# Kernel optimization log

Hardware: AMD Instinct MI355X
Metric: run time of the kernel (lower is better)

## Reference

```python
import jax, jax.numpy as jnp
import numpy as np

NUM_HASHES = 10
GROUP = 2
K = 5


def _strip_att(x, conv_w, rvecs, horizontal):
    # x: [n, c, h, w]; conv_w: [group*k, c]; rvecs: [num_hashes, c]
    n, c, h, w = x.shape
    hw = h * w
    pad = K // 2

    # ---- LSH group selection (vectorized, no python batch loop) ----
    x_flat = x.reshape(n, c, hw).transpose(0, 2, 1)          # [n, hw, c]
    proj = jnp.einsum('ntc,hc->nth', x_flat, rvecs)          # [n, hw, num_hashes]
    codes = (proj > 0).astype(jnp.float32)
    pow2 = jnp.power(2.0, jnp.arange(NUM_HASHES, dtype=jnp.float32))
    dec = codes @ pow2                                       # [n, hw]
    order = jnp.argsort(dec, axis=1)                         # [n, hw]
    sorted_t = jnp.take_along_axis(x_flat, order[:, :, None], axis=1)  # [n, hw, c]

    # select_best_group: batch element with largest L2 norm, shared by all
    norms = jnp.linalg.norm(sorted_t.reshape(n, -1), axis=1)  # [n]
    best = jnp.argmax(norms)
    best_group = jnp.take(sorted_t, best, axis=0)             # [hw, c]
    bg = jnp.broadcast_to(best_group.T.reshape(1, c, h, w), (n, c, h, w))

    # ---- sigmoid-gated dynamic strip filter (1x1 conv) ----
    filt = jnp.einsum('oc,nchw->nohw', conv_w, bg)            # [n, group*K, h, w]
    filt = jax.nn.sigmoid(filt).reshape(n, GROUP, 1, K, hw)

    # ---- unfold (im2col) along the strip axis, reflect-padded ----
    if horizontal:
        xp = jnp.pad(x, ((0, 0), (0, 0), (0, 0), (pad, pad)), mode='reflect')
        windows = jnp.stack([xp[:, :, :, i:i + w] for i in range(K)], axis=2)  # [n,c,K,h,w]
    else:
        xp = jnp.pad(x, ((0, 0), (0, 0), (pad, pad), (0, 0)), mode='reflect')
        windows = jnp.stack([xp[:, :, i:i + h, :] for i in range(K)], axis=2)  # [n,c,K,h,w]
    xr = windows.reshape(n, GROUP, c // GROUP, K, hw)

    out = jnp.sum(xr * filt, axis=3).reshape(n, c, h, w)
    return out


def setup_inputs() -> dict:
    key = jax.random.key(0)
    ks = jax.random.split(key, 7)
    n, c, h, w = 4, 64, 256, 256
    return {
        'x': jax.random.normal(ks[0], (n, c, h, w), dtype=jnp.float32),
        'conv_h_w': jax.random.normal(ks[1], (GROUP * K, c), dtype=jnp.float32) * 0.1,
        'conv_w_w': jax.random.normal(ks[2], (GROUP * K, c), dtype=jnp.float32) * 0.1,
        'rvecs_h': jax.random.normal(ks[3], (NUM_HASHES, c), dtype=jnp.float32),
        'rvecs_w': jax.random.normal(ks[4], (NUM_HASHES, c), dtype=jnp.float32),
        'gamma': jax.random.normal(ks[5], (c,), dtype=jnp.float32),
        'beta': jax.random.normal(ks[6], (c,), dtype=jnp.float32),
    }


def reference(x, conv_h_w, conv_w_w, rvecs_h, rvecs_w, gamma, beta):
    out = _strip_att(x, conv_h_w, rvecs_h, horizontal=True)
    out = _strip_att(out, conv_w_w, rvecs_w, horizontal=False)
    return gamma[None, :, None, None] * out + x * beta[None, :, None, None]
```

## Files before the change

### kernel.cpp

```cpp
#include <hip/hip_runtime.h>

#define NB 4
#define C 64
#define H 256
#define W 256
#define HW (H * W)
#define NH 10
#define KK 5
#define NBINS 1024
#define CHUNK 256
#define NCHUNK (HW / CHUNK)

__global__ __launch_bounds__(256) void sumsq_kernel(const float* __restrict__ x,
                                                    float* __restrict__ part) {
    int bid = blockIdx.x;
    int b = bid >> 8, ch = bid & 255;
    const float4* p = reinterpret_cast<const float4*>(x + (size_t)b * C * HW) + (size_t)ch * 4096;
    float s = 0.f;
    for (int i = threadIdx.x; i < 4096; i += 256) {
        float4 v = p[i];
        s += v.x * v.x + v.y * v.y + v.z * v.z + v.w * v.w;
    }
    __shared__ float red[256];
    red[threadIdx.x] = s;
    __syncthreads();
    for (int off = 128; off; off >>= 1) {
        if (threadIdx.x < off) red[threadIdx.x] += red[threadIdx.x + off];
        __syncthreads();
    }
    if (threadIdx.x == 0) part[bid] = red[0];
}

__global__ __launch_bounds__(256) void hash_kernel(const float* __restrict__ Xall,
                                                   const float* __restrict__ part,
                                                   int per_batch,
                                                   const float* __restrict__ rvecs,
                                                   const float* __restrict__ cwg,
                                                   float* __restrict__ filtU,
                                                   int* __restrict__ dec,
                                                   int* __restrict__ hist) {
    __shared__ float tile[32][CHUNK + 4];
    __shared__ float rv[NH * C];
    __shared__ float cw[NH * C];
    __shared__ int lhist[NBINS];
    __shared__ float4 red4[256];
    int t = threadIdx.x;
    for (int i = t; i < NH * C; i += 256) { rv[i] = rvecs[i]; cw[i] = cwg[i]; }
    for (int i = t; i < NBINS; i += 256) lhist[i] = 0;

    float4 ss = make_float4(0.f, 0.f, 0.f, 0.f);
    int q4 = per_batch >> 2;
    for (int i = t; i < q4; i += 256) {
        float4 a = *reinterpret_cast<const float4*>(part + 0 * per_batch + i * 4);
        float4 b = *reinterpret_cast<const float4*>(part + 1 * per_batch + i * 4);
        float4 c = *reinterpret_cast<const float4*>(part + 2 * per_batch + i * 4);
        float4 d = *reinterpret_cast<const float4*>(part + 3 * per_batch + i * 4);
        ss.x += a.x + a.y + a.z + a.w;
        ss.y += b.x + b.y + b.z + b.w;
        ss.z += c.x + c.y + c.z + c.w;
        ss.w += d.x + d.y + d.z + d.w;
    }
    red4[t] = ss;
    __syncthreads();
    for (int off = 128; off; off >>= 1) {
        if (t < off) {
            red4[t].x += red4[t + off].x;
            red4[t].y += red4[t + off].y;
            red4[t].z += red4[t + off].z;
            red4[t].w += red4[t + off].w;
        }
        __syncthreads();
    }
    float4 nm = red4[0];
    float nv[NB] = {nm.x, nm.y, nm.z, nm.w};
    int best = 0;
    float m = nv[0];
#pragma unroll
    for (int i = 1; i < NB; i++)
        if (nv[i] > m) { m = nv[i]; best = i; }

    const float* X = Xall + (size_t)best * C * HW;
    int p0 = blockIdx.x * CHUNK;
    int lane = t & 63, cq = t >> 6;
    float acc[NH], cacc[NH];
#pragma unroll
    for (int h = 0; h < NH; h++) { acc[h] = 0.f; cacc[h] = 0.f; }

    for (int half = 0; half < 2; half++) {
        __syncthreads();
        const float* Xh = X + (size_t)(half * 32) * HW + p0;
#pragma unroll
        for (int rep = 0; rep < 8; rep++) {
            int cl = rep * 4 + cq;
            float4 v = *reinterpret_cast<const float4*>(Xh + (size_t)cl * HW + lane * 4);
            *reinterpret_cast<float4*>(&tile[cl][lane * 4]) = v;
        }
        __syncthreads();
#pragma unroll
        for (int c = 0; c < 32; c++) {
            float v = tile[c][t];
            int ci = half * 32 + c;
#pragma unroll
            for (int h = 0; h < NH; h++) {
                acc[h] += v * rv[h * C + ci];
                cacc[h] += v * cw[h * C + ci];
            }
        }
    }
    int d = 0;
#pragma unroll
    for (int h = 0; h < NH; h++) d |= (acc[h] > 0.f) ? (1 << h) : 0;
    dec[p0 + t] = d;
    atomicAdd(&lhist[d], 1);

    float sg[NH];
#pragma unroll
    for (int h = 0; h < NH; h++) sg[h] = 1.f / (1.f + expf(-cacc[h]));
    float* fu = filtU + (size_t)(p0 + t) * 12;
    *reinterpret_cast<float4*>(fu + 0) = make_float4(sg[0], sg[1], sg[2], sg[3]);
    *reinterpret_cast<float4*>(fu + 4) = make_float4(sg[4], sg[5], sg[6], sg[7]);
    *reinterpret_cast<float4*>(fu + 8) = make_float4(sg[8], sg[9], 0.f, 0.f);

    __syncthreads();
    for (int i = t; i < NBINS; i += 256) hist[(size_t)i * NCHUNK + blockIdx.x] = lhist[i];
}

__global__ __launch_bounds__(256) void scan1_kernel(int* __restrict__ hist,
                                                    int* __restrict__ bintot) {
    int t = threadIdx.x;
    int lane = t & 63;
    int b = blockIdx.x * 4 + (t >> 6);
    int4 v = *reinterpret_cast<int4*>(hist + (size_t)b * NCHUNK + lane * 4);
    int s0 = v.x, s1 = s0 + v.y, s2 = s1 + v.z, s3 = s2 + v.w;
    int s = s3;
#pragma unroll
    for (int off = 1; off < 64; off <<= 1) {
        int nbr = __shfl_up(s, off);
        if (lane >= off) s += nbr;
    }
    int excl = s - s3;
    int4 o;
    o.x = excl;
    o.y = excl + s0;
    o.z = excl + s1;
    o.w = excl + s2;
    *reinterpret_cast<int4*>(hist + (size_t)b * NCHUNK + lane * 4) = o;
    if (lane == 63) bintot[b] = s;
}

__global__ __launch_bounds__(256) void scatter_kernel(const int* __restrict__ dec,
                                                      const int* __restrict__ hist,
                                                      const int* __restrict__ bintot,
                                                      const float* __restrict__ filtU,
                                                      float* __restrict__ filt) {
    __shared__ int boffs[NBINS];
    __shared__ int wtot[4];
    __shared__ int keys[CHUNK];
    int t = threadIdx.x;
    int lane = t & 63;
    int w = t >> 6;
    int4 v = *reinterpret_cast<const int4*>(bintot + t * 4);
    int s0 = v.x, s1 = s0 + v.y, s2 = s1 + v.z, s3 = s2 + v.w;
    int s = s3;
#pragma unroll
    for (int off = 1; off < 64; off <<= 1) {
        int nbr = __shfl_up(s, off);
        if (lane >= off) s += nbr;
    }
    int excl = s - s3;
    if (lane == 63) wtot[w] = s;
    __syncthreads();
    int wbase = 0;
#pragma unroll
    for (int i = 0; i < 4; i++) wbase += (i < w) ? wtot[i] : 0;
    boffs[t * 4 + 0] = wbase + excl;
    boffs[t * 4 + 1] = wbase + excl + s0;
    boffs[t * 4 + 2] = wbase + excl + s1;
    boffs[t * 4 + 3] = wbase + excl + s2;

    int p0 = blockIdx.x * CHUNK;
    int k = dec[p0 + t];
    keys[t] = k;
    __syncthreads();
    int r = 0;
    for (int j = 0; j < t; j++) r += (keys[j] == k) ? 1 : 0;
    int dst = boffs[k] + hist[(size_t)k * NCHUNK + blockIdx.x] + r;

    const float4* fu = reinterpret_cast<const float4*>(filtU + (size_t)(p0 + t) * 12);
    float4 a = fu[0], b4 = fu[1], c4 = fu[2];
    float vv[10] = {a.x, a.y, a.z, a.w, b4.x, b4.y, b4.z, b4.w, c4.x, c4.y};
#pragma unroll
    for (int h = 0; h < NH; h++) filt[(size_t)h * HW + dst] = vv[h];
}

__global__ __launch_bounds__(256) void convh_kernel(const float* __restrict__ X,
                                                    const float* __restrict__ filt,
                                                    float* __restrict__ out1,
                                                    float* __restrict__ part) {
    int bid = blockIdx.x;
    int rb = bid & 63;
    int c = (bid >> 6) & (C - 1);
    int n = bid >> 12;
    int g = c >> 5;
    int t = threadIdx.x;
    int x4 = (t & 63) * 4;
    int y = rb * 4 + (t >> 6);

    const float* src = X + (((size_t)n * C + c) * H + y) * W;
    float4 M = *reinterpret_cast<const float4*>(src + x4);
    float s0, s1, s6, s7;
    if (x4 > 0) {
        float4 L = *reinterpret_cast<const float4*>(src + x4 - 4);
        s0 = L.z; s1 = L.w;
    } else {
        s0 = M.z; s1 = M.y;
    }
    if (x4 < W - 4) {
        float4 R = *reinterpret_cast<const float4*>(src + x4 + 4);
        s6 = R.x; s7 = R.y;
    } else {
        s6 = M.z; s7 = M.y;
    }
    float s[8] = {s0, s1, M.x, M.y, M.z, M.w, s6, s7};

    const float* fb = filt + (size_t)g * KK * HW + (size_t)y * W + x4;
    float4 acc = make_float4(0.f, 0.f, 0.f, 0.f);
#pragma unroll
    for (int k = 0; k < KK; k++) {
        float4 f = *reinterpret_cast<const float4*>(fb + (size_t)k * HW);
        acc.x += s[k] * f.x;
        acc.y += s[k + 1] * f.y;
        acc.z += s[k + 2] * f.z;
        acc.w += s[k + 3] * f.w;
    }
    *reinterpret_cast<float4*>(out1 + (((size_t)n * C + c) * H + y) * W + x4) = acc;

    float ss = acc.x * acc.x + acc.y * acc.y + acc.z * acc.z + acc.w * acc.w;
#pragma unroll
    for (int off = 32; off; off >>= 1) ss += __shfl_down(ss, off);
    __shared__ float wred[4];
    if ((t & 63) == 0) wred[t >> 6] = ss;
    __syncthreads();
    if (t == 0) part[bid] = wred[0] + wred[1] + wred[2] + wred[3];
}

__global__ __launch_bounds__(256) void convv_kernel(const float* __restrict__ out1,
                                                    const float* __restrict__ filt,
                                                    const float* __restrict__ x,
                                                    const float* __restrict__ gamma,
                                                    const float* __restrict__ beta,
                                                    float* __restrict__ out) {
    int bid = blockIdx.x;
    int yc = bid & 3;
    int c = (bid >> 2) & (C - 1);
    int n = bid >> 8;
    int g = c >> 5;
    int t = threadIdx.x;
    int x4 = (t & 63) * 4;
    int ys = yc * 64 + (t >> 6) * 16;

    const float* plane = out1 + ((size_t)n * C + c) * HW;
    float4 win[KK];
#pragma unroll
    for (int i = 0; i < 4; i++) {
        int yy = ys - 2 + i;
        yy = yy < 0 ? -yy : yy;
        win[i] = *reinterpret_cast<const float4*>(plane + (size_t)yy * W + x4);
    }
    float gm = gamma[c], bt = beta[c];
    const float* fgb = filt + (size_t)g * KK * HW;
    for (int dy = 0; dy < 16; dy++) {
        int y = ys + dy;
        int yy = y + 2;
        yy = (yy >= H) ? (2 * H - 2 - yy) : yy;
        win[4] = *reinterpret_cast<const float4*>(plane + (size_t)yy * W + x4);
        const float* fb = fgb + (size_t)y * W + x4;
        float4 acc = make_float4(0.f, 0.f, 0.f, 0.f);
#pragma unroll
        for (int k = 0; k < KK; k++) {
            float4 f = *reinterpret_cast<const float4*>(fb + (size_t)k * HW);
            acc.x += win[k].x * f.x;
            acc.y += win[k].y * f.y;
            acc.z += win[k].z * f.z;
            acc.w += win[k].w * f.w;
        }
        size_t idx = (((size_t)n * C + c) * H + y) * W + x4;
        float4 xv = *reinterpret_cast<const float4*>(x + idx);
        float4 o;
        o.x = gm * acc.x + bt * xv.x;
        o.y = gm * acc.y + bt * xv.y;
        o.z = gm * acc.z + bt * xv.z;
        o.w = gm * acc.w + bt * xv.w;
        *reinterpret_cast<float4*>(out + idx) = o;
#pragma unroll
        for (int k = 0; k < 4; k++) win[k] = win[k + 1];
    }
}

extern "C" void kernel_launch(void* const* d_in, const int* in_sizes, int n_in,
                              void* d_out, int out_size, void* d_ws, size_t ws_size,
                              hipStream_t stream) {
    const float* x      = (const float*)d_in[0];
    const float* conv_h = (const float*)d_in[1];
    const float* conv_w = (const float*)d_in[2];
    const float* rv_h   = (const float*)d_in[3];
    const float* rv_w   = (const float*)d_in[4];
    const float* gamma  = (const float*)d_in[5];
    const float* beta   = (const float*)d_in[6];
    float* out = (float*)d_out;

    char* w = (char*)d_ws;
    size_t off = 0;
    float* out1   = (float*)(w + off); off += (size_t)NB * C * HW * 4;
    float* filtU  = (float*)(w + off); off += (size_t)HW * 12 * 4;
    float* filt   = (float*)(w + off); off += (size_t)NH * HW * 4;
    int*   dec    = (int*)  (w + off); off += (size_t)HW * 4;
    int*   hist   = (int*)  (w + off); off += (size_t)NBINS * NCHUNK * 4;
    int*   bintot = (int*)  (w + off); off += 4096;
    float* part1  = (float*)(w + off); off += (size_t)NB * 256 * 4;
    float* part2  = (float*)(w + off); off += (size_t)NB * 4096 * 4;

    sumsq_kernel<<<NB * 256, 256, 0, stream>>>(x, part1);
    hash_kernel<<<NCHUNK, 256, 0, stream>>>(x, part1, 256, rv_h, conv_h, filtU, dec, hist);
    scan1_kernel<<<NBINS / 4, 256, 0, stream>>>(hist, bintot);
    scatter_kernel<<<NCHUNK, 256, 0, stream>>>(dec, hist, bintot, filtU, filt);
    convh_kernel<<<NB * C * (H / 4), 256, 0, stream>>>(x, filt, out1, part2);

    hash_kernel<<<NCHUNK, 256, 0, stream>>>(out1, part2, 4096, rv_w, conv_w, filtU, dec, hist);
    scan1_kernel<<<NBINS / 4, 256, 0, stream>>>(hist, bintot);
    scatter_kernel<<<NCHUNK, 256, 0, stream>>>(dec, hist, bintot, filtU, filt);
    convv_kernel<<<NB * C * 4, 256, 0, stream>>>(out1, filt, x, gamma, beta, out);
}
```

Baseline: 145.6 us.

## Fuse all stages into one cooperative persistent kernel with grid syncs

Replaces the nine separate kernel launches with a single cooperative persistent kernel that loops over work units per phase and separates phases with grid-wide barriers. The per-phase bodies become device functions sharing reused shared-memory buffers, and the old launch sequence stays as a fallback. The sumsq and hash tiling are retuned to smaller chunks (2048 sumsq units, 8-channel hash tiles) to fit the shared buffer. The aim is to remove launch gaps between the many small phases. The cost is grid.sync overhead, a grid capped at the occupancy limit, and lower occupancy, since the fused kernel holds the largest shared-memory and register footprint of all phases for the whole run.

After: 430.8 us. +196.0%, slower.

```diff
diff --git a/kernel.cpp b/kernel.cpp
--- a/kernel.cpp
+++ b/kernel.cpp
@@ -1,4 +1,7 @@
 #include <hip/hip_runtime.h>
+#include <hip/hip_cooperative_groups.h>
+
+namespace cg = cooperative_groups;
 
 #define NB 4
 #define C 64
@@ -10,44 +13,32 @@
 #define NBINS 1024
 #define CHUNK 256
 #define NCHUNK (HW / CHUNK)
-
-__global__ __launch_bounds__(256) void sumsq_kernel(const float* __restrict__ x,
-                                                    float* __restrict__ part) {
-    int bid = blockIdx.x;
-    int b = bid >> 8, ch = bid & 255;
-    const float4* p = reinterpret_cast<const float4*>(x + (size_t)b * C * HW) + (size_t)ch * 4096;
+#define MAXGRID 2048
+
+
+__device__ __forceinline__ void sumsq_unit(int u, int t, float* smA,
+                                           const float* __restrict__ x,
+                                           float* __restrict__ part1) {
+    int b = u >> 9, ch = u & 511;
+    const float4* p = reinterpret_cast<const float4*>(x + (size_t)b * C * HW) + (size_t)ch * 2048;
     float s = 0.f;
-    for (int i = threadIdx.x; i < 4096; i += 256) {
+    for (int i = t; i < 2048; i += 256) {
         float4 v = p[i];
         s += v.x * v.x + v.y * v.y + v.z * v.z + v.w * v.w;
     }
-    __shared__ float red[256];
-    red[threadIdx.x] = s;
+    smA[t] = s;
     __syncthreads();
     for (int off = 128; off; off >>= 1) {
-        if (threadIdx.x < off) red[threadIdx.x] += red[threadIdx.x + off];
+        if (t < off) smA[t] += smA[t + off];
         __syncthreads();
     }
-    if (threadIdx.x == 0) part[bid] = red[0];
-}
-
-__global__ __launch_bounds__(256) void hash_kernel(const float* __restrict__ Xall,
-                                                   const float* __restrict__ part,
-                                                   int per_batch,
-                                                   const float* __restrict__ rvecs,
-                                                   const float* __restrict__ cwg,
-                                                   float* __restrict__ filtU,
-                                                   int* __restrict__ dec,
-                                                   int* __restrict__ hist) {
-    __shared__ float tile[32][CHUNK + 4];
-    __shared__ float rv[NH * C];
-    __shared__ float cw[NH * C];
-    __shared__ int lhist[NBINS];
-    __shared__ float4 red4[256];
-    int t = threadIdx.x;
-    for (int i = t; i < NH * C; i += 256) { rv[i] = rvecs[i]; cw[i] = cwg[i]; }
-    for (int i = t; i < NBINS; i += 256) lhist[i] = 0;
-
+    if (t == 0) part1[u] = smA[0];
+    __syncthreads();
+}
+
+__device__ __forceinline__ int block_argmax(int t, float* smA,
+                                            const float* __restrict__ part, int per_batch) {
+    float4* red4 = reinterpret_cast<float4*>(smA);
     float4 ss = make_float4(0.f, 0.f, 0.f, 0.f);
     int q4 = per_batch >> 2;
     for (int i = t; i < q4; i += 256) {
@@ -72,34 +63,49 @@
         __syncthreads();
     }
     float4 nm = red4[0];
+    __syncthreads();
     float nv[NB] = {nm.x, nm.y, nm.z, nm.w};
     int best = 0;
     float m = nv[0];
 #pragma unroll
     for (int i = 1; i < NB; i++)
         if (nv[i] > m) { m = nv[i]; best = i; }
+    return best;
+}
+
+__device__ __forceinline__ void hash_phase(int u, int t, float* smA, float* smB,
+        const float* __restrict__ Xall, const float* __restrict__ part, int per_batch,
+        const float* __restrict__ rvecs, const float* __restrict__ cwg,
+        float* __restrict__ filtU, int* __restrict__ dec, int* __restrict__ hist) {
+    float* rv = smB;
+    float* cw = smB + NH * C;
+    int* lhist = reinterpret_cast<int*>(smB + 2 * NH * C);
+    for (int i = t; i < NH * C; i += 256) { rv[i] = rvecs[i]; cw[i] = cwg[i]; }
+    for (int i = t; i < NBINS; i += 256) lhist[i] = 0;
+    int best = block_argmax(t, smA, part, per_batch);
 
     const float* X = Xall + (size_t)best * C * HW;
-    int p0 = blockIdx.x * CHUNK;
-    int lane = t & 63, cq = t >> 6;
+    int p0 = u * CHUNK;
     float acc[NH], cacc[NH];
 #pragma unroll
     for (int h = 0; h < NH; h++) { acc[h] = 0.f; cacc[h] = 0.f; }
-
-    for (int half = 0; half < 2; half++) {
+    float(*tile)[CHUNK + 4] = reinterpret_cast<float(*)[CHUNK + 4]>(smA);
+    for (int s8 = 0; s8 < 8; s8++) {
         __syncthreads();
-        const float* Xh = X + (size_t)(half * 32) * HW + p0;
-#pragma unroll
-        for (int rep = 0; rep < 8; rep++) {
-            int cl = rep * 4 + cq;
-            float4 v = *reinterpret_cast<const float4*>(Xh + (size_t)cl * HW + lane * 4);
+#pragma unroll
+        for (int k = 0; k < 2; k++) {
+            int idx = t + k * 256;
+            int cl = idx >> 6;
+            int lane = idx & 63;
+            float4 v = *reinterpret_cast<const float4*>(
+                X + (size_t)(s8 * 8 + cl) * HW + p0 + lane * 4);
             *reinterpret_cast<float4*>(&tile[cl][lane * 4]) = v;
         }
         __syncthreads();
 #pragma unroll
-        for (int c = 0; c < 32; c++) {
+        for (int c = 0; c < 8; c++) {
             float v = tile[c][t];
-            int ci = half * 32 + c;
+            int ci = s8 * 8 + c;
 #pragma unroll
             for (int h = 0; h < NH; h++) {
                 acc[h] += v * rv[h * C + ci];
@@ -112,7 +118,6 @@
     for (int h = 0; h < NH; h++) d |= (acc[h] > 0.f) ? (1 << h) : 0;
     dec[p0 + t] = d;
     atomicAdd(&lhist[d], 1);
-
     float sg[NH];
 #pragma unroll
     for (int h = 0; h < NH; h++) sg[h] = 1.f / (1.f + expf(-cacc[h]));
@@ -120,16 +125,15 @@
     *reinterpret_cast<float4*>(fu + 0) = make_float4(sg[0], sg[1], sg[2], sg[3]);
     *reinterpret_cast<float4*>(fu + 4) = make_float4(sg[4], sg[5], sg[6], sg[7]);
     *reinterpret_cast<float4*>(fu + 8) = make_float4(sg[8], sg[9], 0.f, 0.f);
-
-    __syncthreads();
-    for (int i = t; i < NBINS; i += 256) hist[(size_t)i * NCHUNK + blockIdx.x] = lhist[i];
-}
-
-__global__ __launch_bounds__(256) void scan1_kernel(int* __restrict__ hist,
-                                                    int* __restrict__ bintot) {
-    int t = threadIdx.x;
+    __syncthreads();
+    for (int i = t; i < NBINS; i += 256) hist[(size_t)i * NCHUNK + u] = lhist[i];
+    __syncthreads();
+}
+
+__device__ __forceinline__ void scan_phase(int u, int t, int* __restrict__ hist,
+                                           int* __restrict__ bintot) {
     int lane = t & 63;
-    int b = blockIdx.x * 4 + (t >> 6);
+    int b = u * 4 + (t >> 6);
     int4 v = *reinterpret_cast<int4*>(hist + (size_t)b * NCHUNK + lane * 4);
     int s0 = v.x, s1 = s0 + v.y, s2 = s1 + v.z, s3 = s2 + v.w;
     int s = s3;
@@ -148,15 +152,13 @@
     if (lane == 63) bintot[b] = s;
 }
 
-__global__ __launch_bounds__(256) void scatter_kernel(const int* __restrict__ dec,
-                                                      const int* __restrict__ hist,
-                                                      const int* __restrict__ bintot,
-                                                      const float* __restrict__ filtU,
-                                                      float* __restrict__ filt) {
-    __shared__ int boffs[NBINS];
-    __shared__ int wtot[4];
-    __shared__ int keys[CHUNK];
-    int t = threadIdx.x;
+__device__ __forceinline__ void scatter_phase(int u, int t, float* smA,
+        const int* __restrict__ dec, const int* __restrict__ hist,
+        const int* __restrict__ bintot, const float* __restrict__ filtU,
+        float* __restrict__ filt) {
+    int* boffs = reinterpret_cast<int*>(smA);
+    int* wtot = boffs + NBINS;
+    int* keys = wtot + 4;
     int lane = t & 63;
     int w = t >> 6;
     int4 v = *reinterpret_cast<const int4*>(bintot + t * 4);
@@ -178,31 +180,29 @@
     boffs[t * 4 + 2] = wbase + excl + s1;
     boffs[t * 4 + 3] = wbase + excl + s2;
 
-    int p0 = blockIdx.x * CHUNK;
+    int p0 = u * CHUNK;
     int k = dec[p0 + t];
     keys[t] = k;
     __syncthreads();
     int r = 0;
     for (int j = 0; j < t; j++) r += (keys[j] == k) ? 1 : 0;
-    int dst = boffs[k] + hist[(size_t)k * NCHUNK + blockIdx.x] + r;
+    int dst = boffs[k] + hist[(size_t)k * NCHUNK + u] + r;
 
     const float4* fu = reinterpret_cast<const float4*>(filtU + (size_t)(p0 + t) * 12);
     float4 a = fu[0], b4 = fu[1], c4 = fu[2];
     float vv[10] = {a.x, a.y, a.z, a.w, b4.x, b4.y, b4.z, b4.w, c4.x, c4.y};
 #pragma unroll
     for (int h = 0; h < NH; h++) filt[(size_t)h * HW + dst] = vv[h];
-}
-
-__global__ __launch_bounds__(256) void convh_kernel(const float* __restrict__ X,
-                                                    const float* __restrict__ filt,
-                                                    float* __restrict__ out1,
-                                                    float* __restrict__ part) {
-    int bid = blockIdx.x;
-    int rb = bid & 63;
-    int c = (bid >> 6) & (C - 1);
-    int n = bid >> 12;
+    __syncthreads();
+}
+
+__device__ __forceinline__ void convh_unit(int u, int t, float* smA,
+        const float* __restrict__ X, const float* __restrict__ filt,
+        float* __restrict__ out1, float* __restrict__ part2) {
+    int rb = u & 63;
+    int c = (u >> 6) & (C - 1);
+    int n = u >> 12;
     int g = c >> 5;
-    int t = threadIdx.x;
     int x4 = (t & 63) * 4;
     int y = rb * 4 + (t >> 6);
 
@@ -238,24 +238,20 @@
     float ss = acc.x * acc.x + acc.y * acc.y + acc.z * acc.z + acc.w * acc.w;
 #pragma unroll
     for (int off = 32; off; off >>= 1) ss += __shfl_down(ss, off);
-    __shared__ float wred[4];
-    if ((t & 63) == 0) wred[t >> 6] = ss;
-    __syncthreads();
-    if (t == 0) part[bid] = wred[0] + wred[1] + wred[2] + wred[3];
-}
-
-__global__ __launch_bounds__(256) void convv_kernel(const float* __restrict__ out1,
-                                                    const float* __restrict__ filt,
-                                                    const float* __restrict__ x,
-                                                    const float* __restrict__ gamma,
-                                                    const float* __restrict__ beta,
-                                                    float* __restrict__ out) {
-    int bid = blockIdx.x;
-    int yc = bid & 3;
-    int c = (bid >> 2) & (C - 1);
-    int n = bid >> 8;
+    if ((t & 63) == 0) smA[t >> 6] = ss;
+    __syncthreads();
+    if (t == 0) part2[u] = smA[0] + smA[1] + smA[2] + smA[3];
+    __syncthreads();
+}
+
+__device__ __forceinline__ void convv_unit(int u, int t,
+        const float* __restrict__ out1, const float* __restrict__ filt,
+        const float* __restrict__ x, const float* __restrict__ gamma,
+        const float* __restrict__ beta, float* __restrict__ out) {
+    int yc = u & 3;
+    int c = (u >> 2) & (C - 1);
+    int n = u >> 8;
     int g = c >> 5;
-    int t = threadIdx.x;
     int x4 = (t & 63) * 4;
     int ys = yc * 64 + (t >> 6) * 16;
 
@@ -297,6 +293,83 @@
     }
 }
 
+__global__ __launch_bounds__(256) void mega_kernel(
+        const float* __restrict__ x, const float* __restrict__ convh_w,
+        const float* __restrict__ convw_w, const float* __restrict__ rvh,
+        const float* __restrict__ rvw, const float* __restrict__ gamma,
+        const float* __restrict__ beta, float* __restrict__ out,
+        float* __restrict__ out1, float* __restrict__ filtU, float* __restrict__ filt,
+        int* __restrict__ dec, int* __restrict__ hist, int* __restrict__ bintot,
+        float* __restrict__ part1, float* __restrict__ part2) {
+    cg::grid_group grid = cg::this_grid();
+    __shared__ __align__(16) float smA[2080];
+    __shared__ __align__(16) float smB[2304];
+    int t = threadIdx.x;
+    int bid = blockIdx.x;
+    int gd = gridDim.x;
+
+    for (int u = bid; u < 2048; u += gd) sumsq_unit(u, t, smA, x, part1);
+    grid.sync();
+    for (int u = bid; u < NCHUNK; u += gd)
+        hash_phase(u, t, smA, smB, x, part1, 512, rvh, convh_w, filtU, dec, hist);
+    grid.sync();
+    for (int u = bid; u < NBINS / 4; u += gd) scan_phase(u, t, hist, bintot);
+    grid.sync();
+    for (int u = bid; u < NCHUNK; u += gd)
+        scatter_phase(u, t, smA, dec, hist, bintot, filtU, filt);
+    grid.sync();
+    for (int u = bid; u < NB * C * (H / 4); u += gd)
+        convh_unit(u, t, smA, x, filt, out1, part2);
+    grid.sync();
+    for (int u = bid; u < NCHUNK; u += gd)
+        hash_phase(u, t, smA, smB, out1, part2, 4096, rvw, convw_w, filtU, dec, hist);
+    grid.sync();
+    for (int u = bid; u < NBINS / 4; u += gd) scan_phase(u, t, hist, bintot);
+    grid.sync();
+    for (int u = bid; u < NCHUNK; u += gd)
+        scatter_phase(u, t, smA, dec, hist, bintot, filtU, filt);
+    grid.sync();
+    for (int u = bid; u < NB * C * 4; u += gd)
+        convv_unit(u, t, out1, filt, x, gamma, beta, out);
+}
+
+__global__ __launch_bounds__(256) void k_sumsq(const float* __restrict__ x,
+                                               float* __restrict__ part1) {
+    __shared__ __align__(16) float smA[256];
+    sumsq_unit(blockIdx.x, threadIdx.x, smA, x, part1);
+}
+__global__ __launch_bounds__(256) void k_hash(const float* __restrict__ Xall,
+        const float* __restrict__ part, int per_batch, const float* __restrict__ rvecs,
+        const float* __restrict__ cwg, float* __restrict__ filtU,
+        int* __restrict__ dec, int* __restrict__ hist) {
+    __shared__ __align__(16) float smA[2080];
+    __shared__ __align__(16) float smB[2304];
+    hash_phase(blockIdx.x, threadIdx.x, smA, smB, Xall, part, per_batch, rvecs, cwg,
+               filtU, dec, hist);
+}
+__global__ __launch_bounds__(256) void k_scan(int* __restrict__ hist,
+                                              int* __restrict__ bintot) {
+    scan_phase(blockIdx.x, threadIdx.x, hist, bintot);
+}
+__global__ __launch_bounds__(256) void k_scatter(const int* __restrict__ dec,
+        const int* __restrict__ hist, const int* __restrict__ bintot,
+        const float* __restrict__ filtU, float* __restrict__ filt) {
+    __shared__ __align__(16) float smA[1312];
+    scatter_phase(blockIdx.x, threadIdx.x, smA, dec, hist, bintot, filtU, filt);
+}
+__global__ __launch_bounds__(256) void k_convh(const float* __restrict__ X,
+        const float* __restrict__ filt, float* __restrict__ out1,
+        float* __restrict__ part2) {
+    __shared__ __align__(16) float smA[4];
+    convh_unit(blockIdx.x, threadIdx.x, smA, X, filt, out1, part2);
+}
+__global__ __launch_bounds__(256) void k_convv(const float* __restrict__ out1,
+        const float* __restrict__ filt, const float* __restrict__ x,
+        const float* __restrict__ gamma, const float* __restrict__ beta,
+        float* __restrict__ out) {
+    convv_unit(blockIdx.x, threadIdx.x, out1, filt, x, gamma, beta, out);
+}
+
 extern "C" void kernel_launch(void* const* d_in, const int* in_sizes, int n_in,
                               void* d_out, int out_size, void* d_ws, size_t ws_size,
                               hipStream_t stream) {
@@ -317,17 +390,39 @@
     int*   dec    = (int*)  (w + off); off += (size_t)HW * 4;
     int*   hist   = (int*)  (w + off); off += (size_t)NBINS * NCHUNK * 4;
     int*   bintot = (int*)  (w + off); off += 4096;
-    float* part1  = (float*)(w + off); off += (size_t)NB * 256 * 4;
+    float* part1  = (float*)(w + off); off += (size_t)NB * 512 * 4;
     float* part2  = (float*)(w + off); off += (size_t)NB * 4096 * 4;
 
-    sumsq_kernel<<<NB * 256, 256, 0, stream>>>(x, part1);
-    hash_kernel<<<NCHUNK, 256, 0, stream>>>(x, part1, 256, rv_h, conv_h, filtU, dec, hist);
-    scan1_kernel<<<NBINS / 4, 256, 0, stream>>>(hist, bintot);
-    scatter_kernel<<<NCHUNK, 256, 0, stream>>>(dec, hist, bintot, filtU, filt);
-    convh_kernel<<<NB * C * (H / 4), 256, 0, stream>>>(x, filt, out1, part2);
-
-    hash_kernel<<<NCHUNK, 256, 0, stream>>>(out1, part2, 4096, rv_w, conv_w, filtU, dec, hist);
-    scan1_kernel<<<NBINS / 4, 256, 0, stream>>>(hist, bintot);
-    scatter_kernel<<<NCHUNK, 256, 0, stream>>>(dec, hist, bintot, filtU, filt);
-    convv_kernel<<<NB * C * 4, 256, 0, stream>>>(out1, filt, x, gamma, beta, out);
-}
+    int dev = 0;
+    (void)hipGetDevice(&dev);
+    int nMP = 0;
+    (void)hipDeviceGetAttribute(&nMP, hipDeviceAttributeMultiprocessorCount, dev);
+    int bpm = 0;
+    hipError_t oe = hipOccupancyMaxActiveBlocksPerMultiprocessor(&bpm, mega_kernel, 256, 0);
+
+    bool coop_ok = false;
+    if (oe == hipSuccess && nMP > 0 && bpm > 0) {
+        int G = nMP * bpm;
+        if (G > MAXGRID) G = MAXGRID;
+        if (G >= 64) {
+            void* args[] = {&x, &conv_h, &conv_w, &rv_h, &rv_w, &gamma, &beta,
+                            &out, &out1, &filtU, &filt, &dec, &hist, &bintot,
+                            &part1, &part2};
+            hipError_t le = hipLaunchCooperativeKernel(
+                reinterpret_cast<void*>(mega_kernel), dim3(G), dim3(256), args, 0, stream);
+            coop_ok = (le == hipSuccess);
+        }
+    }
+
+    if (!coop_ok) {
+        k_sumsq<<<2048, 256, 0, stream>>>(x, part1);
+        k_hash<<<NCHUNK, 256, 0, stream>>>(x, part1, 512, rv_h, conv_h, filtU, dec, hist);
+        k_scan<<<NBINS / 4, 256, 0, stream>>>(hist, bintot);
+        k_scatter<<<NCHUNK, 256, 0, stream>>>(dec, hist, bintot, filtU, filt);
+        k_convh<<<NB * C * (H / 4), 256, 0, stream>>>(x, filt, out1, part2);
+        k_hash<<<NCHUNK, 256, 0, stream>>>(out1, part2, 4096, rv_w, conv_w, filtU, dec, hist);
+        k_scan<<<NBINS / 4, 256, 0, stream>>>(hist, bintot);
+        k_scatter<<<NCHUNK, 256, 0, stream>>>(dec, hist, bintot, filtU, filt);
+        k_convv<<<NB * C * 4, 256, 0, stream>>>(out1, filt, x, gamma, beta, out);
+    }
+}
```

## Split hash projection across 1024 threads and use ballot-based stable rank in scatter

Applied to the files above, without the earlier changes.

The hash kernel now uses 1024-thread blocks. Each quarter of the threads projects 16 channels per pixel, and the partial sums are reduced through shared memory. The scatter kernel replaces its O(n) linear scan for stable rank with per-wave ballot matching on the 10 key bits plus per-wave shared histograms. The sumsq kernel is split into twice as many blocks. These changes target the long serial loops in the hash and scatter kernels, at the cost of more shared-memory traffic and barriers in the hash reduction.

Result: faster. 139.3 us (-4.3%).

```diff
diff --git a/kernel.cpp b/kernel.cpp
--- a/kernel.cpp
+++ b/kernel.cpp
@@ -11,46 +11,43 @@
 #define CHUNK 256
 #define NCHUNK (HW / CHUNK)
 
-__global__ __launch_bounds__(256) void sumsq_kernel(const float* __restrict__ x,
-                                                    float* __restrict__ part) {
-    int bid = blockIdx.x;
-    int b = bid >> 8, ch = bid & 255;
-    const float4* p = reinterpret_cast<const float4*>(x + (size_t)b * C * HW) + (size_t)ch * 4096;
+__global__ __launch_bounds__(256) void k_sumsq(const float* __restrict__ x,
+                                               float* __restrict__ part1) {
+    __shared__ float red[256];
+    int u = blockIdx.x, t = threadIdx.x;
+    int b = u >> 9, ch = u & 511;
+    const float4* p = reinterpret_cast<const float4*>(x + (size_t)b * C * HW) + (size_t)ch * 2048;
     float s = 0.f;
-    for (int i = threadIdx.x; i < 4096; i += 256) {
+    for (int i = t; i < 2048; i += 256) {
         float4 v = p[i];
         s += v.x * v.x + v.y * v.y + v.z * v.z + v.w * v.w;
     }
-    __shared__ float red[256];
-    red[threadIdx.x] = s;
+    red[t] = s;
     __syncthreads();
     for (int off = 128; off; off >>= 1) {
-        if (threadIdx.x < off) red[threadIdx.x] += red[threadIdx.x + off];
+        if (t < off) red[t] += red[t + off];
         __syncthreads();
     }
-    if (threadIdx.x == 0) part[bid] = red[0];
-}
-
-__global__ __launch_bounds__(256) void hash_kernel(const float* __restrict__ Xall,
-                                                   const float* __restrict__ part,
-                                                   int per_batch,
-                                                   const float* __restrict__ rvecs,
-                                                   const float* __restrict__ cwg,
-                                                   float* __restrict__ filtU,
-                                                   int* __restrict__ dec,
-                                                   int* __restrict__ hist) {
-    __shared__ float tile[32][CHUNK + 4];
-    __shared__ float rv[NH * C];
-    __shared__ float cw[NH * C];
+    if (t == 0) part1[u] = red[0];
+}
+
+__global__ __launch_bounds__(1024) void k_hash(const float* __restrict__ Xall,
+                                               const float* __restrict__ part,
+                                               int per_batch,
+                                               const float* __restrict__ rvecs,
+                                               const float* __restrict__ cwg,
+                                               float* __restrict__ filtU,
+                                               int* __restrict__ dec,
+                                               int* __restrict__ hist) {
+    __shared__ __align__(16) float smbuf[256 * 21];
     __shared__ int lhist[NBINS];
-    __shared__ float4 red4[256];
     int t = threadIdx.x;
-    for (int i = t; i < NH * C; i += 256) { rv[i] = rvecs[i]; cw[i] = cwg[i]; }
-    for (int i = t; i < NBINS; i += 256) lhist[i] = 0;
-
+    for (int i = t; i < NBINS; i += 1024) lhist[i] = 0;
+
+    float4* red4 = reinterpret_cast<float4*>(smbuf);
     float4 ss = make_float4(0.f, 0.f, 0.f, 0.f);
     int q4 = per_batch >> 2;
-    for (int i = t; i < q4; i += 256) {
+    for (int i = t; i < q4; i += 1024) {
         float4 a = *reinterpret_cast<const float4*>(part + 0 * per_batch + i * 4);
         float4 b = *reinterpret_cast<const float4*>(part + 1 * per_batch + i * 4);
         float4 c = *reinterpret_cast<const float4*>(part + 2 * per_batch + i * 4);
@@ -62,7 +59,7 @@
     }
     red4[t] = ss;
     __syncthreads();
-    for (int off = 128; off; off >>= 1) {
+    for (int off = 512; off; off >>= 1) {
         if (t < off) {
             red4[t].x += red4[t + off].x;
             red4[t].y += red4[t + off].y;
@@ -72,6 +69,7 @@
         __syncthreads();
     }
     float4 nm = red4[0];
+    __syncthreads();
     float nv[NB] = {nm.x, nm.y, nm.z, nm.w};
     int best = 0;
     float m = nv[0];
@@ -79,54 +77,67 @@
     for (int i = 1; i < NB; i++)
         if (nv[i] > m) { m = nv[i]; best = i; }
 
-    const float* X = Xall + (size_t)best * C * HW;
+    int pix = t & 255;
+    int q = t >> 8;
     int p0 = blockIdx.x * CHUNK;
-    int lane = t & 63, cq = t >> 6;
+    const float* X = Xall + (size_t)best * C * HW + p0 + pix;
+
+    float v[16];
+#pragma unroll
+    for (int k = 0; k < 16; k++) v[k] = X[(size_t)(q * 16 + k) * HW];
+
     float acc[NH], cacc[NH];
 #pragma unroll
     for (int h = 0; h < NH; h++) { acc[h] = 0.f; cacc[h] = 0.f; }
-
-    for (int half = 0; half < 2; half++) {
+#pragma unroll
+    for (int k = 0; k < 16; k++) {
+        int ci = q * 16 + k;
+#pragma unroll
+        for (int h = 0; h < NH; h++) {
+            acc[h] += v[k] * rvecs[h * C + ci];
+            cacc[h] += v[k] * cwg[h * C + ci];
+        }
+    }
+
+    for (int qq = 1; qq < 4; qq++) {
         __syncthreads();
-        const float* Xh = X + (size_t)(half * 32) * HW + p0;
-#pragma unroll
-        for (int rep = 0; rep < 8; rep++) {
-            int cl = rep * 4 + cq;
-            float4 v = *reinterpret_cast<const float4*>(Xh + (size_t)cl * HW + lane * 4);
-            *reinterpret_cast<float4*>(&tile[cl][lane * 4]) = v;
+        if (q == qq) {
+#pragma unroll
+            for (int h = 0; h < NH; h++) {
+                smbuf[pix * 21 + h] = acc[h];
+                smbuf[pix * 21 + 10 + h] = cacc[h];
+            }
         }
         __syncthreads();
-#pragma unroll
-        for (int c = 0; c < 32; c++) {
-            float v = tile[c][t];
-            int ci = half * 32 + c;
+        if (q == 0) {
 #pragma unroll
             for (int h = 0; h < NH; h++) {
-                acc[h] += v * rv[h * C + ci];
-                cacc[h] += v * cw[h * C + ci];
+                acc[h] += smbuf[pix * 21 + h];
+                cacc[h] += smbuf[pix * 21 + 10 + h];
             }
         }
     }
-    int d = 0;
-#pragma unroll
-    for (int h = 0; h < NH; h++) d |= (acc[h] > 0.f) ? (1 << h) : 0;
-    dec[p0 + t] = d;
-    atomicAdd(&lhist[d], 1);
-
-    float sg[NH];
-#pragma unroll
-    for (int h = 0; h < NH; h++) sg[h] = 1.f / (1.f + expf(-cacc[h]));
-    float* fu = filtU + (size_t)(p0 + t) * 12;
-    *reinterpret_cast<float4*>(fu + 0) = make_float4(sg[0], sg[1], sg[2], sg[3]);
-    *reinterpret_cast<float4*>(fu + 4) = make_float4(sg[4], sg[5], sg[6], sg[7]);
-    *reinterpret_cast<float4*>(fu + 8) = make_float4(sg[8], sg[9], 0.f, 0.f);
-
-    __syncthreads();
-    for (int i = t; i < NBINS; i += 256) hist[(size_t)i * NCHUNK + blockIdx.x] = lhist[i];
-}
-
-__global__ __launch_bounds__(256) void scan1_kernel(int* __restrict__ hist,
-                                                    int* __restrict__ bintot) {
+
+    if (q == 0) {
+        int d = 0;
+#pragma unroll
+        for (int h = 0; h < NH; h++) d |= (acc[h] > 0.f) ? (1 << h) : 0;
+        dec[p0 + pix] = d;
+        atomicAdd(&lhist[d], 1);
+        float sg[NH];
+#pragma unroll
+        for (int h = 0; h < NH; h++) sg[h] = 1.f / (1.f + expf(-cacc[h]));
+        float* fu = filtU + (size_t)(p0 + pix) * 12;
+        *reinterpret_cast<float4*>(fu + 0) = make_float4(sg[0], sg[1], sg[2], sg[3]);
+        *reinterpret_cast<float4*>(fu + 4) = make_float4(sg[4], sg[5], sg[6], sg[7]);
+        *reinterpret_cast<float4*>(fu + 8) = make_float4(sg[8], sg[9], 0.f, 0.f);
+    }
+    __syncthreads();
+    for (int i = t; i < NBINS; i += 1024) hist[(size_t)i * NCHUNK + blockIdx.x] = lhist[i];
+}
+
+__global__ __launch_bounds__(256) void k_scan(int* __restrict__ hist,
+                                              int* __restrict__ bintot) {
     int t = threadIdx.x;
     int lane = t & 63;
     int b = blockIdx.x * 4 + (t >> 6);
@@ -148,17 +159,22 @@
     if (lane == 63) bintot[b] = s;
 }
 
-__global__ __launch_bounds__(256) void scatter_kernel(const int* __restrict__ dec,
-                                                      const int* __restrict__ hist,
-                                                      const int* __restrict__ bintot,
-                                                      const float* __restrict__ filtU,
-                                                      float* __restrict__ filt) {
+__global__ __launch_bounds__(256) void k_scatter(const int* __restrict__ dec,
+                                                 const int* __restrict__ hist,
+                                                 const int* __restrict__ bintot,
+                                                 const float* __restrict__ filtU,
+                                                 float* __restrict__ filt) {
     __shared__ int boffs[NBINS];
     __shared__ int wtot[4];
-    __shared__ int keys[CHUNK];
+    __shared__ int lhw[4][NBINS];
     int t = threadIdx.x;
     int lane = t & 63;
     int w = t >> 6;
+    for (int i = t; i < 4 * NBINS; i += 256) (&lhw[0][0])[i] = 0;
+
+    int p0 = blockIdx.x * CHUNK;
+    int k = dec[p0 + t];
+
     int4 v = *reinterpret_cast<const int4*>(bintot + t * 4);
     int s0 = v.x, s1 = s0 + v.y, s2 = s1 + v.z, s3 = s2 + v.w;
     int s = s3;
@@ -178,12 +194,20 @@
     boffs[t * 4 + 2] = wbase + excl + s1;
     boffs[t * 4 + 3] = wbase + excl + s2;
 
-    int p0 = blockIdx.x * CHUNK;
-    int k = dec[p0 + t];
-    keys[t] = k;
-    __syncthreads();
-    int r = 0;
-    for (int j = 0; j < t; j++) r += (keys[j] == k) ? 1 : 0;
+    atomicAdd(&lhw[w][k], 1);
+    unsigned long long msk = ~0ull;
+#pragma unroll
+    for (int b = 0; b < 10; b++) {
+        int bit = (k >> b) & 1;
+        unsigned long long bb = __ballot(bit);
+        msk &= bit ? bb : ~bb;
+    }
+    int rin = __popcll(msk & ((1ull << lane) - 1ull));
+    __syncthreads();
+
+    int r = rin;
+#pragma unroll
+    for (int w2 = 0; w2 < 3; w2++) r += (w2 < w) ? lhw[w2][k] : 0;
     int dst = boffs[k] + hist[(size_t)k * NCHUNK + blockIdx.x] + r;
 
     const float4* fu = reinterpret_cast<const float4*>(filtU + (size_t)(p0 + t) * 12);
@@ -193,16 +217,16 @@
     for (int h = 0; h < NH; h++) filt[(size_t)h * HW + dst] = vv[h];
 }
 
-__global__ __launch_bounds__(256) void convh_kernel(const float* __restrict__ X,
-                                                    const float* __restrict__ filt,
-                                                    float* __restrict__ out1,
-                                                    float* __restrict__ part) {
-    int bid = blockIdx.x;
-    int rb = bid & 63;
-    int c = (bid >> 6) & (C - 1);
-    int n = bid >> 12;
+__global__ __launch_bounds__(256) void k_convh(const float* __restrict__ X,
+                                               const float* __restrict__ filt,
+                                               float* __restrict__ out1,
+                                               float* __restrict__ part2) {
+    __shared__ float wred[4];
+    int u = blockIdx.x, t = threadIdx.x;
+    int rb = u & 63;
+    int c = (u >> 6) & (C - 1);
+    int n = u >> 12;
     int g = c >> 5;
-    int t = threadIdx.x;
     int x4 = (t & 63) * 4;
     int y = rb * 4 + (t >> 6);
 
@@ -238,24 +262,22 @@
     float ss = acc.x * acc.x + acc.y * acc.y + acc.z * acc.z + acc.w * acc.w;
 #pragma unroll
     for (int off = 32; off; off >>= 1) ss += __shfl_down(ss, off);
-    __shared__ float wred[4];
     if ((t & 63) == 0) wred[t >> 6] = ss;
     __syncthreads();
-    if (t == 0) part[bid] = wred[0] + wred[1] + wred[2] + wred[3];
-}
-
-__global__ __launch_bounds__(256) void convv_kernel(const float* __restrict__ out1,
-                                                    const float* __restrict__ filt,
-                                                    const float* __restrict__ x,
-                                                    const float* __restrict__ gamma,
-                                                    const float* __restrict__ beta,
-                                                    float* __restrict__ out) {
-    int bid = blockIdx.x;
-    int yc = bid & 3;
-    int c = (bid >> 2) & (C - 1);
-    int n = bid >> 8;
+    if (t == 0) part2[u] = wred[0] + wred[1] + wred[2] + wred[3];
+}
+
+__global__ __launch_bounds__(256) void k_convv(const float* __restrict__ out1,
+                                               const float* __restrict__ filt,
+                                               const float* __restrict__ x,
+                                               const float* __restrict__ gamma,
+                                               const float* __restrict__ beta,
+                                               float* __restrict__ out) {
+    int u = blockIdx.x, t = threadIdx.x;
+    int yc = u & 3;
+    int c = (u >> 2) & (C - 1);
+    int n = u >> 8;
     int g = c >> 5;
-    int t = threadIdx.x;
     int x4 = (t & 63) * 4;
     int ys = yc * 64 + (t >> 6) * 16;
 
@@ -317,17 +339,17 @@
     int*   dec    = (int*)  (w + off); off += (size_t)HW * 4;
     int*   hist   = (int*)  (w + off); off += (size_t)NBINS * NCHUNK * 4;
     int*   bintot = (int*)  (w + off); off += 4096;
-    float* part1  = (float*)(w + off); off += (size_t)NB * 256 * 4;
+    float* part1  = (float*)(w + off); off += (size_t)NB * 512 * 4;
     float* part2  = (float*)(w + off); off += (size_t)NB * 4096 * 4;
 
-    sumsq_kernel<<<NB * 256, 256, 0, stream>>>(x, part1);
-    hash_kernel<<<NCHUNK, 256, 0, stream>>>(x, part1, 256, rv_h, conv_h, filtU, dec, hist);
-    scan1_kernel<<<NBINS / 4, 256, 0, stream>>>(hist, bintot);
-    scatter_kernel<<<NCHUNK, 256, 0, stream>>>(dec, hist, bintot, filtU, filt);
-    convh_kernel<<<NB * C * (H / 4), 256, 0, stream>>>(x, filt, out1, part2);
-
-    hash_kernel<<<NCHUNK, 256, 0, stream>>>(out1, part2, 4096, rv_w, conv_w, filtU, dec, hist);
-    scan1_kernel<<<NBINS / 4, 256, 0, stream>>>(hist, bintot);
-    scatter_kernel<<<NCHUNK, 256, 0, stream>>>(dec, hist, bintot, filtU, filt);
-    convv_kernel<<<NB * C * 4, 256, 0, stream>>>(out1, filt, x, gamma, beta, out);
-}
+    k_sumsq<<<2048, 256, 0, stream>>>(x, part1);
+    k_hash<<<NCHUNK, 1024, 0, stream>>>(x, part1, 512, rv_h, conv_h, filtU, dec, hist);
+    k_scan<<<NBINS / 4, 256, 0, stream>>>(hist, bintot);
+    k_scatter<<<NCHUNK, 256, 0, stream>>>(dec, hist, bintot, filtU, filt);
+    k_convh<<<NB * C * (H / 4), 256, 0, stream>>>(x, filt, out1, part2);
+
+    k_hash<<<NCHUNK, 1024, 0, stream>>>(out1, part2, 4096, rv_w, conv_w, filtU, dec, hist);
+    k_scan<<<NBINS / 4, 256, 0, stream>>>(hist, bintot);
+    k_scatter<<<NCHUNK, 256, 0, stream>>>(dec, hist, bintot, filtU, filt);
+    k_convv<<<NB * C * 4, 256, 0, stream>>>(out1, filt, x, gamma, beta, out);
+}
```
